# Kernel tuning notes

Measured on AMD Instinct MI355X. Metric: run time of the kernel, lower is better.

The kernel has to match this reference:

```python
import jax, jax.numpy as jnp
import numpy as np

N_HEADS = 8
N_POINTS = 4


def _bilinear_sample(vl, g, Hl, Wl):
    # vl: [B, nH, Hl*Wl, hd] level values; g: [B, Q, nH, P, 2] sampling locs in [0,1] (x, y)
    # Emulates torch grid_sample(mode='bilinear', padding_mode='zeros', align_corners=False)
    B, Q, nH, P, _ = g.shape
    hd = vl.shape[-1]
    x = g[..., 0] * Wl - 0.5
    y = g[..., 1] * Hl - 0.5
    x0f = jnp.floor(x)
    y0f = jnp.floor(y)
    x0 = x0f.astype(jnp.int32)
    y0 = y0f.astype(jnp.int32)
    wx1 = x - x0f
    wy1 = y - y0f

    def corner(xi, yi, w):
        valid = (xi >= 0) & (xi < Wl) & (yi >= 0) & (yi < Hl)
        idx = jnp.clip(yi, 0, Hl - 1) * Wl + jnp.clip(xi, 0, Wl - 1)  # [B,Q,nH,P]
        idx = idx.transpose(0, 2, 1, 3).reshape(B, nH, Q * P)
        gathered = jnp.take_along_axis(vl, idx[..., None], axis=2)  # [B,nH,Q*P,hd]
        wm = (w * valid.astype(w.dtype)).transpose(0, 2, 1, 3).reshape(B, nH, Q * P)
        return gathered * wm[..., None]

    s = (corner(x0, y0, (1.0 - wx1) * (1.0 - wy1))
         + corner(x0 + 1, y0, wx1 * (1.0 - wy1))
         + corner(x0, y0 + 1, (1.0 - wx1) * wy1)
         + corner(x0 + 1, y0 + 1, wx1 * wy1))
    return s.reshape(B, nH, Q, P, hd)


def setup_inputs() -> dict:
    key = jax.random.key(0)
    ks = jax.random.split(key, 12)
    B, Q, D = 32, 300, 256
    L, P, nH = 4, N_POINTS, N_HEADS
    shapes = np.array([[80, 80], [40, 40], [20, 20], [10, 10]], dtype=np.int32)
    V = int((shapes[:, 0] * shapes[:, 1]).sum())  # 8500
    lsi = np.concatenate([[0], np.cumsum(shapes[:, 0] * shapes[:, 1])[:-1]]).astype(np.int32)
    sd = 1.0 / np.sqrt(D)
    return {
        'query': jax.random.normal(ks[0], (B, Q, D), jnp.float32),
        'reference_points': jax.random.uniform(ks[1], (B, Q, L, 2), jnp.float32),
        'value': jax.random.normal(ks[2], (B, V, D), jnp.float32),
        'spatial_shapes': jnp.asarray(shapes),
        'level_start_index': jnp.asarray(lsi),
        'W_off': jax.random.normal(ks[3], (D, nH * L * P * 2), jnp.float32) * sd,
        'b_off': jax.random.normal(ks[4], (nH * L * P * 2,), jnp.float32) * 0.5,
        'W_attn': jax.random.normal(ks[5], (D, nH * L * P), jnp.float32) * sd,
        'b_attn': jax.random.normal(ks[6], (nH * L * P,), jnp.float32) * 0.1,
        'W_val': jax.random.normal(ks[7], (D, D), jnp.float32) * sd,
        'b_val': jnp.zeros((D,), jnp.float32),
        'W_out': jax.random.normal(ks[8], (D, D), jnp.float32) * sd,
        'b_out': jnp.zeros((D,), jnp.float32),
    }


def reference(query, reference_points, value, spatial_shapes, level_start_index,
              W_off, b_off, W_attn, b_attn, W_val, b_val, W_out, b_out):
    shapes = np.asarray(spatial_shapes)  # static level shapes
    B, Q, D = query.shape
    nH, P = N_HEADS, N_POINTS
    L = shapes.shape[0]
    hd = D // nH

    val = value @ W_val + b_val  # [B,V,D]
    val = val.reshape(B, -1, nH, hd).transpose(0, 2, 1, 3)  # [B,nH,V,hd]

    off = (query @ W_off + b_off).reshape(B, Q, nH, L, P, 2)
    attn = jax.nn.softmax((query @ W_attn + b_attn).reshape(B, Q, nH, L * P), axis=-1)
    attn = attn.reshape(B, Q, nH, L, P)

    # normalizer is (W_l, H_l)
    norm = jnp.asarray(np.stack([shapes[:, 1], shapes[:, 0]], -1), jnp.float32)  # [L,2]
    loc = reference_points[:, :, None, :, None, :] + off / norm[None, None, None, :, None, :]

    out = jnp.zeros((B, Q, nH, hd), query.dtype)
    start = 0
    for lvl in range(L):
        Hl, Wl = int(shapes[lvl, 0]), int(shapes[lvl, 1])
        vl = val[:, :, start:start + Hl * Wl, :]  # [B,nH,HW,hd]
        sampled = _bilinear_sample(vl, loc[:, :, :, lvl], Hl, Wl)  # [B,nH,Q,P,hd]
        out = out + jnp.einsum('bnqpd,bqnp->bqnd', sampled, attn[:, :, :, lvl])
        start += Hl * Wl

    return out.reshape(B, Q, D) @ W_out + b_out
```

## Files before the change

### kernel.cpp

```cpp
#include <hip/hip_runtime.h>
#include <hip/hip_bf16.h>
#include <math.h>
#include <stdint.h>

#define NB 32
#define NQ 300
#define ND 256
#define NH 8
#define HD 32
#define NL 4
#define NP 4
#define V_TOT 8500
#define BQ_TOT (NB*NQ)
#define MVAL (NB*V_TOT)
#define NOA 384

typedef short v8s __attribute__((ext_vector_type(8)));
typedef float v4f __attribute__((ext_vector_type(4)));

#define AS1 __attribute__((address_space(1)))
#define AS3 __attribute__((address_space(3)))

__device__ __forceinline__ void copy16_async(const void* g, void* l) {
#if __has_builtin(__builtin_amdgcn_global_load_lds)
    __builtin_amdgcn_global_load_lds((const AS1 unsigned int*)g,
                                     (AS3 unsigned int*)l, 16, 0, 0);
#else
    *(uint4*)l = *(const uint4*)g;
#endif
}

__device__ __forceinline__ unsigned short f2bf_rne(float x) {
    unsigned u = __float_as_uint(x);
    u += 0x7fffu + ((u >> 16) & 1u);
    return (unsigned short)(u >> 16);
}
__device__ __forceinline__ float bf2f(unsigned short b) {
    return __uint_as_float(((unsigned)b) << 16);
}

__device__ __forceinline__ void split2(float f0, float f1,
                                       unsigned& hp, unsigned& lp) {
    float2 v; v.x = f0; v.y = f1;
    __hip_bfloat162 h = __float22bfloat162_rn(v);
    unsigned hu; __builtin_memcpy(&hu, &h, 4);
    const float h0 = __uint_as_float(hu << 16);
    const float h1 = __uint_as_float(hu & 0xffff0000u);
    float2 l; l.x = f0 - h0; l.y = f1 - h1;
    __hip_bfloat162 lo = __float22bfloat162_rn(l);
    unsigned lu; __builtin_memcpy(&lu, &lo, 4);
    hp = hu; lp = lu;
}

__device__ __forceinline__ int swz_pos(int n, int k) {
    const int base = k & ~31;
    const int o = (k >> 3) & 3;
    const int op = o ^ ((n >> 1) & 3);
    return n * 256 + base + (op << 3) + (k & 7);
}

__global__ __launch_bounds__(256) void prep_weights(
    const float* __restrict__ W_val, const float* __restrict__ W_off,
    const float* __restrict__ W_attn, const float* __restrict__ W_out,
    const float* __restrict__ b_off, const float* __restrict__ b_attn,
    unsigned short* __restrict__ Bval_h, unsigned short* __restrict__ Bval_l,
    unsigned short* __restrict__ Boa_h,  unsigned short* __restrict__ Boa_l,
    unsigned short* __restrict__ Bout_h, unsigned short* __restrict__ Bout_l,
    float* __restrict__ b_oa)
{
    const int t = blockIdx.x * 256 + threadIdx.x;
    if (t < 65536) {
        const int n = t >> 8, k = t & 255;
        const float x = W_val[k * 256 + n];
        const unsigned short hi = f2bf_rne(x);
        const unsigned short lo = f2bf_rne(x - bf2f(hi));
        const int p = swz_pos(n, k);
        Bval_h[p] = hi; Bval_l[p] = lo;
    } else if (t < 65536 + 98304) {
        const int t2 = t - 65536;
        const int n = t2 >> 8, k = t2 & 255;
        const float x = (n < 256) ? W_off[k * 256 + n] : W_attn[k * 128 + (n - 256)];
        const unsigned short hi = f2bf_rne(x);
        const unsigned short lo = f2bf_rne(x - bf2f(hi));
        const int p = swz_pos(n, k);
        Boa_h[p] = hi; Boa_l[p] = lo;
    } else if (t < 229376) {
        const int t3 = t - 163840;
        const int n = t3 >> 8, k = t3 & 255;
        const float x = W_out[k * 256 + n];
        const unsigned short hi = f2bf_rne(x);
        const unsigned short lo = f2bf_rne(x - bf2f(hi));
        const int p = swz_pos(n, k);
        Bout_h[p] = hi; Bout_l[p] = lo;
    } else {
        const int t4 = t - 229376;
        if (t4 < NOA) b_oa[t4] = (t4 < 256) ? b_off[t4] : b_attn[t4 - 256];
    }
}

__global__ __launch_bounds__(256, 3) void gemm_a32(
    const float* __restrict__ A,
    const unsigned short* __restrict__ Bh,
    const unsigned short* __restrict__ Bl,
    const float* __restrict__ bias,
    float* __restrict__ Cf,
    unsigned short* __restrict__ Cb,
    int ldc, int mode)
{
    __shared__ unsigned short Ah[128][32];
    __shared__ unsigned short Al[128][32];
    __shared__ unsigned short Bs[2][128][32];

    const int tid  = threadIdx.x;
    const int col0 = blockIdx.x * 128;
    const int row0 = blockIdx.y * 128;
    const int wave = tid >> 6;
    const int lane = tid & 63;
    const int wm   = (wave >> 1) * 64;
    const int wn   = (wave & 1) * 64;
    const int m16  = lane & 15;
    const int quad = lane >> 4;

    const int i0  = tid;
    const int i1  = tid + 256;
    const int r0_ = i0 >> 2, o0_ = i0 & 3;
    const int r1_ = i1 >> 2, o1_ = i1 & 3;
    const int oo0 = (o0_ ^ ((r0_ >> 1) & 3)) << 3;
    const int oo1 = (o1_ ^ ((r1_ >> 1) & 3)) << 3;
    const float* Ap0 = A + (size_t)(row0 + r0_) * 256 + o0_ * 8;
    const float* Ap1 = A + (size_t)(row0 + r1_) * 256 + o1_ * 8;

    const int lin0 = (wave * 2 + 0) * 1024 + lane * 16;
    const int lin1 = (wave * 2 + 1) * 1024 + lane * 16;
    const char* pBh0 = (const char*)Bh + ((size_t)(col0 + (lin0 >> 6)) * 256) * 2 + (lin0 & 63);
    const char* pBl0 = (const char*)Bl + ((size_t)(col0 + (lin0 >> 6)) * 256) * 2 + (lin0 & 63);
    const char* pBh1 = (const char*)Bh + ((size_t)(col0 + (lin1 >> 6)) * 256) * 2 + (lin1 & 63);
    const char* pBl1 = (const char*)Bl + ((size_t)(col0 + (lin1 >> 6)) * 256) * 2 + (lin1 & 63);
    char* lBh0 = (char*)&Bs[0][0][0] + lin0;
    char* lBh1 = (char*)&Bs[0][0][0] + lin1;
    char* lBl0 = (char*)&Bs[1][0][0] + lin0;
    char* lBl1 = (char*)&Bs[1][0][0] + lin1;

    v4f acc[4][4] = {};

    float4 f00 = *(const float4*)(Ap0);
    float4 f01 = *(const float4*)(Ap0 + 4);
    float4 f10 = *(const float4*)(Ap1);
    float4 f11 = *(const float4*)(Ap1 + 4);

#pragma unroll
    for (int t = 0; t < 8; ++t) {
        asm volatile("s_waitcnt lgkmcnt(0)" ::: "memory");
        __builtin_amdgcn_s_barrier();

        copy16_async(pBh0 + t * 64, lBh0);
        copy16_async(pBh1 + t * 64, lBh1);
        copy16_async(pBl0 + t * 64, lBl0);
        copy16_async(pBl1 + t * 64, lBl1);

        asm volatile("" ::: "memory");
        __builtin_amdgcn_sched_barrier(0);

        unsigned hpk0[4], lpk0[4], hpk1[4], lpk1[4];
        split2(f00.x, f00.y, hpk0[0], lpk0[0]);
        split2(f00.z, f00.w, hpk0[1], lpk0[1]);
        split2(f01.x, f01.y, hpk0[2], lpk0[2]);
        split2(f01.z, f01.w, hpk0[3], lpk0[3]);
        split2(f10.x, f10.y, hpk1[0], lpk1[0]);
        split2(f10.z, f10.w, hpk1[1], lpk1[1]);
        split2(f11.x, f11.y, hpk1[2], lpk1[2]);
        split2(f11.z, f11.w, hpk1[3], lpk1[3]);

        if (t < 7) {
            const int k1 = (t + 1) * 32;
            f00 = *(const float4*)(Ap0 + k1);
            f01 = *(const float4*)(Ap0 + k1 + 4);
            f10 = *(const float4*)(Ap1 + k1);
            f11 = *(const float4*)(Ap1 + k1 + 4);
        }

        *(uint4*)&Ah[r0_][oo0] = make_uint4(hpk0[0], hpk0[1], hpk0[2], hpk0[3]);
        *(uint4*)&Al[r0_][oo0] = make_uint4(lpk0[0], lpk0[1], lpk0[2], lpk0[3]);
        *(uint4*)&Ah[r1_][oo1] = make_uint4(hpk1[0], hpk1[1], hpk1[2], hpk1[3]);
        *(uint4*)&Al[r1_][oo1] = make_uint4(lpk1[0], lpk1[1], lpk1[2], lpk1[3]);

        if (t < 7) {
            asm volatile("s_waitcnt vmcnt(4) lgkmcnt(0)" ::: "memory");
        } else {
            asm volatile("s_waitcnt vmcnt(0) lgkmcnt(0)" ::: "memory");
        }
        __builtin_amdgcn_s_barrier();

#pragma unroll
        for (int i = 0; i < 4; ++i) {
            const int r  = wm + i * 16 + m16;
            const int ka = (quad ^ ((r >> 1) & 3)) << 3;
            const v8s ah = *(v8s*)&Ah[r][ka];
            const v8s al = *(v8s*)&Al[r][ka];
#pragma unroll
            for (int j = 0; j < 4; ++j) {
                const int n  = wn + j * 16 + m16;
                const int ko = (quad ^ ((n >> 1) & 3)) << 3;
                const v8s bh = *(v8s*)&Bs[0][n][ko];
                const v8s bl = *(v8s*)&Bs[1][n][ko];
                acc[i][j] = __builtin_amdgcn_mfma_f32_16x16x32_bf16(ah, bh, acc[i][j], 0, 0, 0);
                acc[i][j] = __builtin_amdgcn_mfma_f32_16x16x32_bf16(ah, bl, acc[i][j], 0, 0, 0);
                acc[i][j] = __builtin_amdgcn_mfma_f32_16x16x32_bf16(al, bh, acc[i][j], 0, 0, 0);
            }
        }
    }

#pragma unroll
    for (int j = 0; j < 4; ++j) {
        const int cl = col0 + wn + j * 16 + m16;
        const float bb = bias[cl];
        if (mode == 0) {
#pragma unroll
            for (int i = 0; i < 4; ++i)
#pragma unroll
                for (int r = 0; r < 4; ++r) {
                    const int R = row0 + wm + i * 16 + quad * 4 + r;
                    Cf[(size_t)R * ldc + cl] = acc[i][j][r] + bb;
                }
        } else {
            const int h  = cl >> 5;
            const int dh = cl & 31;
#pragma unroll
            for (int i = 0; i < 4; ++i)
#pragma unroll
                for (int r = 0; r < 4; ++r) {
                    const int R = row0 + wm + i * 16 + quad * 4 + r;
                    const unsigned b = (unsigned)R / V_TOT;
                    const int v = R - (int)b * V_TOT;
                    Cb[(((size_t)(b * NH + h)) * V_TOT + v) * HD + dh] =
                        f2bf_rne(acc[i][j][r] + bb);
                }
        }
    }
}

__global__ __launch_bounds__(256) void gemm_a16(
    const unsigned short* __restrict__ A,
    const unsigned short* __restrict__ Bh,
    const unsigned short* __restrict__ Bl,
    const float* __restrict__ bias,
    float* __restrict__ C, int ldc)
{
    __shared__ unsigned short As[2][128][32];
    __shared__ unsigned short Bs[2][2][128][32];

    const int tid  = threadIdx.x;
    const int row0 = blockIdx.x * 128;
    const int col0 = blockIdx.y * 128;
    const int wave = tid >> 6;
    const int lane = tid & 63;
    const int wm   = (wave >> 1) * 64;
    const int wn   = (wave & 1) * 64;
    const int m16  = lane & 15;
    const int quad = lane >> 4;

    v4f acc[4][4] = {};

#pragma unroll
    for (int c = 0; c < 2; ++c) {
        const int linear = (wave * 2 + c) * 1024 + lane * 16;
        const int n   = linear >> 6;
        const int off = linear & 63;
        copy16_async((const char*)A  + ((size_t)(row0 + n) * 256 + 0) * 2 + off,
                     (char*)&As[0][0][0] + linear);
        copy16_async((const char*)Bh + ((size_t)(col0 + n) * 256 + 0) * 2 + off,
                     (char*)&Bs[0][0][0][0] + linear);
        copy16_async((const char*)Bl + ((size_t)(col0 + n) * 256 + 0) * 2 + off,
                     (char*)&Bs[0][1][0][0] + linear);
    }
    __syncthreads();

    for (int t = 0; t < 8; ++t) {
        const int buf = t & 1;
        const int nb  = buf ^ 1;
        const int k1  = (t + 1) << 5;

        if (t < 7) {
#pragma unroll
            for (int c = 0; c < 2; ++c) {
                const int linear = (wave * 2 + c) * 1024 + lane * 16;
                const int n   = linear >> 6;
                const int off = linear & 63;
                copy16_async((const char*)A  + ((size_t)(row0 + n) * 256 + k1) * 2 + off,
                             (char*)&As[nb][0][0] + linear);
                copy16_async((const char*)Bh + ((size_t)(col0 + n) * 256 + k1) * 2 + off,
                             (char*)&Bs[nb][0][0][0] + linear);
                copy16_async((const char*)Bl + ((size_t)(col0 + n) * 256 + k1) * 2 + off,
                             (char*)&Bs[nb][1][0][0] + linear);
            }
        }

        v8s a[4], bh[4], bl[4];
#pragma unroll
        for (int i = 0; i < 4; ++i) {
            const int r  = wm + i * 16 + m16;
            const int ka = (quad ^ ((r >> 1) & 3)) << 3;
            a[i] = *(v8s*)&As[buf][r][ka];
            const int n  = wn + i * 16 + m16;
            const int kb = (quad ^ ((n >> 1) & 3)) << 3;
            bh[i] = *(v8s*)&Bs[buf][0][n][kb];
            bl[i] = *(v8s*)&Bs[buf][1][n][kb];
        }
#pragma unroll
        for (int i = 0; i < 4; ++i)
#pragma unroll
            for (int j = 0; j < 4; ++j) {
                acc[i][j] = __builtin_amdgcn_mfma_f32_16x16x32_bf16(a[i], bh[j], acc[i][j], 0, 0, 0);
                acc[i][j] = __builtin_amdgcn_mfma_f32_16x16x32_bf16(a[i], bl[j], acc[i][j], 0, 0, 0);
            }

        __syncthreads();
    }

#pragma unroll
    for (int j = 0; j < 4; ++j) {
        const int cl = col0 + wn + j * 16 + m16;
        const float bb = bias[cl];
#pragma unroll
        for (int i = 0; i < 4; ++i)
#pragma unroll
            for (int r = 0; r < 4; ++r) {
                const int R = row0 + wm + i * 16 + quad * 4 + r;
                C[(size_t)R * ldc + cl] = acc[i][j][r] + bb;
            }
    }
}

__global__ __launch_bounds__(256) void sample_kernel(
    const float* __restrict__ refp,
    const float* __restrict__ offattn,
    const unsigned short* __restrict__ val,
    unsigned short* __restrict__ pre)
{
    const int t  = blockIdx.x * 256 + threadIdx.x;
    const int d8 = t & 3;
    const int h  = (t >> 2) & 7;
    const int bq = t >> 5;
    const int b  = bq / NQ;

    const float* rp = refp + (size_t)bq * 8;
    const float* op = offattn + (size_t)bq * 384 + h * 32;
    const float* ap = offattn + (size_t)bq * 384 + 256 + h * 16;

    float aw[16];
    float m = -1e30f;
#pragma unroll
    for (int i = 0; i < 16; ++i) { aw[i] = ap[i]; m = fmaxf(m, aw[i]); }
    float s = 0.f;
#pragma unroll
    for (int i = 0; i < 16; ++i) { aw[i] = __expf(aw[i] - m); s += aw[i]; }
    const float inv = 1.f / s;
#pragma unroll
    for (int i = 0; i < 16; ++i) aw[i] *= inv;

    const int Hs[4] = {80, 40, 20, 10};
    const int St[4] = {0, 6400, 8000, 8400};

    float acc[8] = {};
#pragma unroll
    for (int l = 0; l < NL; ++l) {
        const int Wl = Hs[l], Hl = Hs[l];
        const float fW = (float)Wl, fH = (float)Hl;
        const float rx = rp[l * 2 + 0];
        const float ry = rp[l * 2 + 1];
        const unsigned short* vb =
            val + (((size_t)(b * NH + h)) * V_TOT + St[l]) * HD + d8 * 8;
#pragma unroll
        for (int p = 0; p < NP; ++p) {
            const float ox = op[l * 8 + p * 2 + 0];
            const float oy = op[l * 8 + p * 2 + 1];
            const float w  = aw[l * 4 + p];
            const float x = fmaf(rx, fW, ox) - 0.5f;
            const float y = fmaf(ry, fH, oy) - 0.5f;
            const float x0f = floorf(x), y0f = floorf(y);
            const int   x0 = (int)x0f,  y0 = (int)y0f;
            const float wx1 = x - x0f,  wy1 = y - y0f;
            const float wx0 = 1.f - wx1, wy0 = 1.f - wy1;
#pragma unroll
            for (int cy = 0; cy < 2; ++cy) {
#pragma unroll
                for (int cx = 0; cx < 2; ++cx) {
                    const int xi = x0 + cx;
                    const int yi = y0 + cy;
                    float cw = (cx ? wx1 : wx0) * (cy ? wy1 : wy0) * w;
                    const bool valid = (xi >= 0) && (xi < Wl) && (yi >= 0) && (yi < Hl);
                    cw = valid ? cw : 0.f;
                    const int xc = xi < 0 ? 0 : (xi > Wl - 1 ? Wl - 1 : xi);
                    const int yc = yi < 0 ? 0 : (yi > Hl - 1 ? Hl - 1 : yi);
                    const uint4 g = *(const uint4*)(vb + (size_t)(yc * Wl + xc) * HD);
                    const unsigned gu[4] = {g.x, g.y, g.z, g.w};
#pragma unroll
                    for (int e = 0; e < 4; ++e) {
                        acc[2*e]   = fmaf(cw, __uint_as_float(gu[e] << 16),        acc[2*e]);
                        acc[2*e+1] = fmaf(cw, __uint_as_float(gu[e] & 0xffff0000u), acc[2*e+1]);
                    }
                }
            }
        }
    }

    unsigned o[4];
#pragma unroll
    for (int e = 0; e < 4; ++e)
        o[e] = (unsigned)f2bf_rne(acc[2*e]) | ((unsigned)f2bf_rne(acc[2*e+1]) << 16);
    const int octswz = d8 ^ ((bq >> 1) & 3);
    *(uint4*)(pre + (size_t)bq * 256 + h * 32 + octswz * 8) =
        make_uint4(o[0], o[1], o[2], o[3]);
}

extern "C" void kernel_launch(void* const* d_in, const int* in_sizes, int n_in,
                              void* d_out, int out_size, void* d_ws, size_t ws_size,
                              hipStream_t stream)
{
    const float* query  = (const float*)d_in[0];
    const float* refp   = (const float*)d_in[1];
    const float* value  = (const float*)d_in[2];
    const float* W_off  = (const float*)d_in[5];
    const float* b_off  = (const float*)d_in[6];
    const float* W_attn = (const float*)d_in[7];
    const float* b_attn = (const float*)d_in[8];
    const float* W_val  = (const float*)d_in[9];
    const float* b_val  = (const float*)d_in[10];
    const float* W_out  = (const float*)d_in[11];
    const float* b_out  = (const float*)d_in[12];
    float* out = (float*)d_out;

    char* ws = (char*)d_ws;
    unsigned short* val     = (unsigned short*)ws;
    float*          offattn = (float*)(ws + 139264000);
    unsigned short* pre     = (unsigned short*)(ws + 154009600);
    unsigned short* Bval_h  = (unsigned short*)(ws + 158924800);
    unsigned short* Bval_l  = Bval_h + 65536;
    unsigned short* Boa_h   = Bval_l + 65536;
    unsigned short* Boa_l   = Boa_h + 98304;
    unsigned short* Bout_h  = Boa_l + 98304;
    unsigned short* Bout_l  = Bout_h + 65536;
    float*          b_oa    = (float*)(Bout_l + 65536);

    const dim3 blk(256);

    prep_weights<<<dim3(898), blk, 0, stream>>>(
        W_val, W_off, W_attn, W_out, b_off, b_attn,
        Bval_h, Bval_l, Boa_h, Boa_l, Bout_h, Bout_l, b_oa);

    gemm_a32<<<dim3(2, MVAL / 128), blk, 0, stream>>>(
        value, Bval_h, Bval_l, b_val, nullptr, val, 0, 1);

    gemm_a32<<<dim3(3, BQ_TOT / 128), blk, 0, stream>>>(
        query, Boa_h, Boa_l, b_oa, offattn, nullptr, NOA, 0);

    sample_kernel<<<dim3((BQ_TOT * 32) / 256), blk, 0, stream>>>(
        refp, offattn, val, pre);

    gemm_a16<<<dim3(BQ_TOT / 128, 2), blk, 0, stream>>>(
        pre, Bout_h, Bout_l, b_out, out, 256);
}
```

Baseline: 566.8 us.

## Split sampling levels across two half-warps and remap blocks across XCDs

The sampling kernel now launches twice as many threads. Each half of a 64-lane wave handles two of the four pyramid levels, and the partial sums are combined with a cross-half shuffle before one half writes the output. Block indices are also permuted ((g&7)*300 + g>>3) so consecutive hardware block IDs map to contiguous chunks per XCD, which should improve L2 locality of value gathers. The goal is more memory-level parallelism for the latency-bound gathers. The cost is duplicated softmax and address setup per thread, and unbalanced work between the halves, since levels 0 and 1 are heavier only in cache footprint.

```diff
diff --git a/kernel.cpp b/kernel.cpp
--- a/kernel.cpp
+++ b/kernel.cpp
@@ -337,11 +337,14 @@
     const unsigned short* __restrict__ val,
     unsigned short* __restrict__ pre)
 {
-    const int t  = blockIdx.x * 256 + threadIdx.x;
-    const int d8 = t & 3;
-    const int h  = (t >> 2) & 7;
-    const int bq = t >> 5;
-    const int b  = bq / NQ;
+    const int g  = blockIdx.x;
+    const int sb = (g & 7) * 300 + (g >> 3);
+    const int t  = sb * 256 + threadIdx.x;
+    const int d8   = t & 3;
+    const int h    = (t >> 2) & 7;
+    const int half = (t >> 5) & 1;
+    const int bq   = t >> 6;
+    const int b    = bq / NQ;
 
     const float* rp = refp + (size_t)bq * 8;
     const float* op = offattn + (size_t)bq * 384 + h * 32;
@@ -358,23 +361,22 @@
 #pragma unroll
     for (int i = 0; i < 16; ++i) aw[i] *= inv;
 
-    const int Hs[4] = {80, 40, 20, 10};
-    const int St[4] = {0, 6400, 8000, 8400};
-
     float acc[8] = {};
 #pragma unroll
-    for (int l = 0; l < NL; ++l) {
-        const int Wl = Hs[l], Hl = Hs[l];
-        const float fW = (float)Wl, fH = (float)Hl;
-        const float rx = rp[l * 2 + 0];
-        const float ry = rp[l * 2 + 1];
+    for (int li = 0; li < 2; ++li) {
+        const int Wl = li ? (half ? 10 : 40) : (half ? 20 : 80);
+        const int St = li ? (half ? 8400 : 6400) : (half ? 8000 : 0);
+        const int l2 = (half ? 2 : 0) + li;
+        const float fW = (float)Wl, fH = (float)Wl;
+        const float rx = rp[l2 * 2 + 0];
+        const float ry = rp[l2 * 2 + 1];
         const unsigned short* vb =
-            val + (((size_t)(b * NH + h)) * V_TOT + St[l]) * HD + d8 * 8;
+            val + (((size_t)(b * NH + h)) * V_TOT + St) * HD + d8 * 8;
 #pragma unroll
         for (int p = 0; p < NP; ++p) {
-            const float ox = op[l * 8 + p * 2 + 0];
-            const float oy = op[l * 8 + p * 2 + 1];
-            const float w  = aw[l * 4 + p];
+            const float ox = op[l2 * 8 + p * 2 + 0];
+            const float oy = op[l2 * 8 + p * 2 + 1];
+            const float w  = half ? aw[8 + li * 4 + p] : aw[li * 4 + p];
             const float x = fmaf(rx, fW, ox) - 0.5f;
             const float y = fmaf(ry, fH, oy) - 0.5f;
             const float x0f = floorf(x), y0f = floorf(y);
@@ -388,12 +390,12 @@
                     const int xi = x0 + cx;
                     const int yi = y0 + cy;
                     float cw = (cx ? wx1 : wx0) * (cy ? wy1 : wy0) * w;
-                    const bool valid = (xi >= 0) && (xi < Wl) && (yi >= 0) && (yi < Hl);
+                    const bool valid = (xi >= 0) && (xi < Wl) && (yi >= 0) && (yi < Wl);
                     cw = valid ? cw : 0.f;
                     const int xc = xi < 0 ? 0 : (xi > Wl - 1 ? Wl - 1 : xi);
-                    const int yc = yi < 0 ? 0 : (yi > Hl - 1 ? Hl - 1 : yi);
-                    const uint4 g = *(const uint4*)(vb + (size_t)(yc * Wl + xc) * HD);
-                    const unsigned gu[4] = {g.x, g.y, g.z, g.w};
+                    const int yc = yi < 0 ? 0 : (yi > Wl - 1 ? Wl - 1 : yi);
+                    const uint4 gld = *(const uint4*)(vb + (size_t)(yc * Wl + xc) * HD);
+                    const unsigned gu[4] = {gld.x, gld.y, gld.z, gld.w};
 #pragma unroll
                     for (int e = 0; e < 4; ++e) {
                         acc[2*e]   = fmaf(cw, __uint_as_float(gu[e] << 16),        acc[2*e]);
@@ -404,13 +406,18 @@
         }
     }
 
-    unsigned o[4];
-#pragma unroll
-    for (int e = 0; e < 4; ++e)
-        o[e] = (unsigned)f2bf_rne(acc[2*e]) | ((unsigned)f2bf_rne(acc[2*e+1]) << 16);
-    const int octswz = d8 ^ ((bq >> 1) & 3);
-    *(uint4*)(pre + (size_t)bq * 256 + h * 32 + octswz * 8) =
-        make_uint4(o[0], o[1], o[2], o[3]);
+#pragma unroll
+    for (int e = 0; e < 8; ++e) acc[e] += __shfl_xor(acc[e], 32);
+
+    if (half == 0) {
+        unsigned o[4];
+#pragma unroll
+        for (int e = 0; e < 4; ++e)
+            o[e] = (unsigned)f2bf_rne(acc[2*e]) | ((unsigned)f2bf_rne(acc[2*e+1]) << 16);
+        const int octswz = d8 ^ ((bq >> 1) & 3);
+        *(uint4*)(pre + (size_t)bq * 256 + h * 32 + octswz * 8) =
+            make_uint4(o[0], o[1], o[2], o[3]);
+    }
 }
 
 extern "C" void kernel_launch(void* const* d_in, const int* in_sizes, int n_in,
@@ -454,7 +461,7 @@
     gemm_a32<<<dim3(3, BQ_TOT / 128), blk, 0, stream>>>(
         query, Boa_h, Boa_l, b_oa, offattn, nullptr, NOA, 0);
 
-    sample_kernel<<<dim3((BQ_TOT * 32) / 256), blk, 0, stream>>>(
+    sample_kernel<<<dim3((BQ_TOT * 64) / 256), blk, 0, stream>>>(
         refp, offattn, val, pre);
 
     gemm_a16<<<dim3(BQ_TOT / 128, 2), blk, 0, stream>>>(
```

New measurement: 531.3 us. -6.3%, faster.
